# Kernel tuning notes

Hardware: AMD Instinct MI355X
Metric: run time of the kernel (lower is better)

## Reference

```python
import jax, jax.numpy as jnp
import numpy as np

D_MODEL = 1024
N_HEADS = 16
HEAD_DIM = D_MODEL // N_HEADS


def setup_inputs() -> dict:
    key = jax.random.key(0)
    k1, k2, k3 = jax.random.split(key, 3)
    B, S = 4, 2048
    x = jax.random.normal(k1, (B, S, D_MODEL), dtype=jnp.float32)
    # scaled init so logits stay reasonable
    w_qkv = jax.random.normal(k2, (D_MODEL, 3 * D_MODEL), dtype=jnp.float32) / np.sqrt(D_MODEL)
    b_qkv = jnp.zeros((3 * D_MODEL,), dtype=jnp.float32)
    w_out = jax.random.normal(k3, (D_MODEL, D_MODEL), dtype=jnp.float32) / np.sqrt(D_MODEL)
    b_out = jnp.zeros((D_MODEL,), dtype=jnp.float32)
    return {"x": x, "w_qkv": w_qkv, "b_qkv": b_qkv, "w_out": w_out, "b_out": b_out}


def reference(x, w_qkv, b_qkv, w_out, b_out):
    B, S, D = x.shape
    qkv = x @ w_qkv + b_qkv                      # [B,S,3D]
    q, k, v = jnp.split(qkv, 3, axis=-1)
    def split_heads(t):
        return t.reshape(B, S, N_HEADS, HEAD_DIM).transpose(0, 2, 1, 3)  # [B,H,S,d]
    q, k, v = split_heads(q), split_heads(k), split_heads(v)
    a = jnp.einsum('bhsd,bhtd->bhst', q, k)      # [B,H,S,S]
    # causal mask added BEFORE scaling, as in the original module
    causal_mask = jnp.triu(jnp.full((S, S), -jnp.inf, dtype=a.dtype), k=1)
    a = (a + causal_mask) / np.sqrt(HEAD_DIM)
    a = jax.nn.softmax(a, axis=-1)
    z = jnp.einsum('bhst,bhtd->bhsd', a, v)      # [B,H,S,d]
    z = z.transpose(0, 2, 1, 3).reshape(B, S, D)
    return z @ w_out + b_out
```

## Files before the change

### kernel.cpp

```cpp
#include <hip/hip_runtime.h>
#include <hip/hip_bf16.h>
#include <stdint.h>

#define B_   4
#define S_   2048
#define H_   16
#define HD_  64
#define D_   1024

typedef short  short8  __attribute__((ext_vector_type(8)));
typedef float  f32x4   __attribute__((ext_vector_type(4)));
typedef float  f32x16  __attribute__((ext_vector_type(16)));

__device__ __forceinline__ unsigned short f2bf(float f) {
    union { float f; unsigned u; } v; v.f = f;
    unsigned r = v.u + 0x7fffu + ((v.u >> 16) & 1u);
    return (unsigned short)(r >> 16);
}

#if __has_builtin(__builtin_amdgcn_exp2f)
#define EXP2(x) __builtin_amdgcn_exp2f(x)
#else
#define EXP2(x) exp2f(x)
#endif

__device__ __forceinline__ unsigned cvtpk(float lo, float hi) {
    unsigned r;
    asm("v_cvt_pk_bf16_f32 %0, %1, %2" : "=v"(r) : "v"(lo), "v"(hi));
    return r;
}

__device__ __forceinline__ float bq(float v, int srclane) {
    return __int_as_float(__builtin_amdgcn_ds_bpermute(srclane << 2, __float_as_int(v)));
}

__device__ __forceinline__ void pl32swap(unsigned &x, unsigned &y) {
    asm volatile("v_permlane32_swap_b32 %0, %1" : "+v"(x), "+v"(y));
}

#define MFMA32(a, b, c) __builtin_amdgcn_mfma_f32_32x32x16_bf16(a, b, c, 0, 0, 0)
#define MFMA16(a, b, c) __builtin_amdgcn_mfma_f32_16x16x32_bf16(a, b, c, 0, 0, 0)

__global__ __launch_bounds__(256) void k_cvt(const float* __restrict__ in,
                                             unsigned short* __restrict__ out) {
    int i = (blockIdx.x * 256 + threadIdx.x) * 4;
    float4 f = *(const float4*)(in + i);
    ushort4 o;
    o.x = f2bf(f.x); o.y = f2bf(f.y); o.z = f2bf(f.z); o.w = f2bf(f.w);
    *(ushort4*)(out + i) = o;
}

__global__ __launch_bounds__(256) void k_transpose_cvt(const float* __restrict__ in,
                                                       unsigned short* __restrict__ out,
                                                       int K, int N) {
    __shared__ float tile[32][33];
    int n0 = blockIdx.x * 32, k0 = blockIdx.y * 32;
    int tx = threadIdx.x, ty = threadIdx.y;
#pragma unroll
    for (int i = 0; i < 32; i += 8)
        tile[ty + i][tx] = in[(size_t)(k0 + ty + i) * N + n0 + tx];
    __syncthreads();
#pragma unroll
    for (int i = 0; i < 32; i += 8)
        out[(size_t)(n0 + ty + i) * K + k0 + tx] = f2bf(tile[tx][ty + i]);
}

__device__ __forceinline__ void async_load16(const unsigned short* g, unsigned short* l) {
    __builtin_amdgcn_global_load_lds(
        (const __attribute__((address_space(1))) unsigned int*)g,
        (__attribute__((address_space(3))) unsigned int*)l, 16, 0, 0);
}

template <int TPOSED>
__global__ __launch_bounds__(512, 1) void k_gemm8(const unsigned short* __restrict__ A,
                                                  const unsigned short* __restrict__ BT,
                                                  const float* __restrict__ bias,
                                                  unsigned short* __restrict__ qb,
                                                  unsigned short* __restrict__ kb,
                                                  unsigned short* __restrict__ vtb,
                                                  int M, int N, int K, int nbase) {
    __shared__ __attribute__((aligned(16))) unsigned short A0s[256 * 64];
    __shared__ __attribute__((aligned(16))) unsigned short A1s[256 * 64];
    __shared__ __attribute__((aligned(16))) unsigned short A2s[256 * 64];
    __shared__ __attribute__((aligned(16))) unsigned short W0s[128 * 64];
    __shared__ __attribute__((aligned(16))) unsigned short W1s[128 * 64];
    __shared__ __attribute__((aligned(16))) unsigned short W2s[128 * 64];
    const int tid = threadIdx.x, wave = tid >> 6, lane = tid & 63;
    const int wR = wave >> 2, wC = wave & 3;
    const int m0 = blockIdx.y * 256, n0 = nbase + blockIdx.x * 128;

    const unsigned short* AG = A + (size_t)m0 * K;
    const unsigned short* WG = BT + (size_t)n0 * K;

    const int rbase = wave * 8 + (lane >> 3);
    const int scol8 = ((lane & 7) ^ ((lane >> 3) & 7)) * 8;
    const int sdst  = wave * 512;
    const int q15 = lane & 15, q4 = (lane >> 4) << 2;
    const int cb0 = ((lane >> 4) * 16) ^ ((lane & 7) << 4);
    const int cb1 = (64 + (lane >> 4) * 16) ^ ((lane & 7) << 4);

    f32x4 acc[2][4][2] = {};

#define STAGE3(SA, SW, KT, KH)                                                        \
    if ((KH) == 0) {                                                                  \
        async_load16(AG + (size_t)(rbase)       * K + (KT) + scol8, (SA) + 0 * 4096 + sdst); \
        async_load16(AG + (size_t)(64 + rbase)  * K + (KT) + scol8, (SA) + 1 * 4096 + sdst); \
        async_load16(WG + (size_t)(rbase)       * K + (KT) + scol8, (SW) + 0 * 4096 + sdst); \
    } else {                                                                          \
        async_load16(AG + (size_t)(128 + rbase) * K + (KT) + scol8, (SA) + 2 * 4096 + sdst); \
        async_load16(AG + (size_t)(192 + rbase) * K + (KT) + scol8, (SA) + 3 * 4096 + sdst); \
        async_load16(WG + (size_t)(64 + rbase)  * K + (KT) + scol8, (SW) + 1 * 4096 + sdst); \
    }

#define PHASEBODY(CA, CW, SA, SW, MORE, KT2, KH, CB)                                  \
    {                                                                                 \
        short8 xf[2][4], yf[2][2];                                                    \
        if (TPOSED) {                                                                 \
            _Pragma("unroll")                                                         \
            for (int i = 0; i < 4; ++i)                                               \
                xf[0][i] = *(const short8*)((const char*)(CW) + (wR * 64 + i * 16 + q15) * 128 + (CB)); \
            _Pragma("unroll")                                                         \
            for (int h = 0; h < 2; ++h)                                               \
                _Pragma("unroll")                                                     \
                for (int j = 0; j < 2; ++j)                                           \
                    yf[h][j] = *(const short8*)((const char*)(CA) + (h * 128 + wC * 32 + j * 16 + q15) * 128 + (CB)); \
        } else {                                                                      \
            _Pragma("unroll")                                                         \
            for (int h = 0; h < 2; ++h)                                               \
                _Pragma("unroll")                                                     \
                for (int i = 0; i < 4; ++i)                                           \
                    xf[h][i] = *(const short8*)((const char*)(CA) + (h * 128 + wR * 64 + i * 16 + q15) * 128 + (CB)); \
            _Pragma("unroll")                                                         \
            for (int j = 0; j < 2; ++j)                                               \
                yf[0][j] = *(const short8*)((const char*)(CW) + (wC * 32 + j * 16 + q15) * 128 + (CB)); \
        }                                                                             \
        if (MORE) {                                                                   \
            STAGE3(SA, SW, KT2, KH)                                                   \
            asm volatile("s_waitcnt vmcnt(6)" ::: "memory");                          \
        } else {                                                                      \
            asm volatile("s_waitcnt vmcnt(0)" ::: "memory");                          \
        }                                                                             \
        __builtin_amdgcn_s_barrier();                                                 \
        asm volatile("s_waitcnt lgkmcnt(0)" ::: "memory");                            \
        __builtin_amdgcn_sched_barrier(0);                                            \
        __builtin_amdgcn_s_setprio(1);                                                \
        _Pragma("unroll")                                                             \
        for (int h = 0; h < 2; ++h)                                                   \
            _Pragma("unroll")                                                         \
            for (int i = 0; i < 4; ++i)                                               \
                _Pragma("unroll")                                                     \
                for (int j = 0; j < 2; ++j)                                           \
                    acc[h][i][j] = MFMA16(TPOSED ? xf[0][i] : xf[h][i],               \
                                          TPOSED ? yf[h][j] : yf[0][j],               \
                                          acc[h][i][j]);                              \
        __builtin_amdgcn_s_setprio(0);                                                \
        asm volatile("" ::: "memory");                                                \
        __builtin_amdgcn_s_barrier();                                                 \
    }

#define TILEBODY(CA, CW, SA, SW, TC)                                                  \
    {                                                                                 \
        const int more_ = ((TC) + 2) < 16;                                            \
        const int kt2_ = ((TC) + 2) * 64;                                             \
        PHASEBODY(CA, CW, SA, SW, more_, kt2_, 0, cb0)                                \
        PHASEBODY(CA, CW, SA, SW, more_, kt2_, 1, cb1)                                \
    }

    STAGE3(A0s, W0s, 0, 0)
    STAGE3(A0s, W0s, 0, 1)
    STAGE3(A1s, W1s, 64, 0)
    STAGE3(A1s, W1s, 64, 1)
    asm volatile("s_waitcnt vmcnt(6)" ::: "memory");
    __builtin_amdgcn_s_barrier();

    for (int t = 0; t < 15; t += 3) {
        TILEBODY(A0s, W0s, A2s, W2s, t)
        TILEBODY(A1s, W1s, A0s, W0s, t + 1)
        TILEBODY(A2s, W2s, A1s, W1s, t + 2)
    }
    TILEBODY(A0s, W0s, A2s, W2s, 15)
#undef STAGE3
#undef PHASEBODY
#undef TILEBODY

    if (TPOSED) {
        unsigned short* dst = (n0 < 1024) ? qb : kb;
        const float scale = (n0 < 1024) ? 0.18033688011112042f : 1.0f;
#pragma unroll
        for (int i = 0; i < 4; ++i) {
            int nr = n0 + wR * 64 + i * 16 + q4;
            float4 bv4 = *(const float4*)(bias + nr);
            int d0 = nr & 63, hh = (nr & 1023) >> 6;
#pragma unroll
            for (int h = 0; h < 2; ++h)
#pragma unroll
            for (int j = 0; j < 2; ++j) {
                int mc = m0 + h * 128 + wC * 32 + j * 16 + q15;
                int b = mc >> 11, s = mc & 2047;
                size_t bh = (size_t)(b * 16 + hh);
                f32x4 a = acc[h][i][j];
                ushort4 o;
                o.x = f2bf((a[0] + bv4.x) * scale);
                o.y = f2bf((a[1] + bv4.y) * scale);
                o.z = f2bf((a[2] + bv4.z) * scale);
                o.w = f2bf((a[3] + bv4.w) * scale);
                size_t off = bh * 131072 +
                    (size_t)((s >> 5) * 4 + (d0 >> 4)) * 512 +
                    ((s & 31) * 2 + ((d0 >> 3) & 1)) * 8 + (d0 & 7);
                *(ushort4*)(dst + off) = o;
            }
        }
    } else {
#pragma unroll
        for (int h = 0; h < 2; ++h)
#pragma unroll
        for (int i = 0; i < 4; ++i) {
            int mr = m0 + h * 128 + wR * 64 + i * 16 + q4;
            int b = mr >> 11, s0 = mr & 2047;
#pragma unroll
            for (int j = 0; j < 2; ++j) {
                int nc = n0 + wC * 32 + j * 16 + q15;
                int rem = nc & 1023, hh = rem >> 6, d = rem & 63;
                float bv = bias[nc];
                f32x4 a = acc[h][i][j];
                ushort4 o;
                o.x = f2bf(a[0] + bv);
                o.y = f2bf(a[1] + bv);
                o.z = f2bf(a[2] + bv);
                o.w = f2bf(a[3] + bv);
                size_t bh = (size_t)(b * 16 + hh);
                size_t off = bh * 131072 +
                    (size_t)((s0 >> 5) * 4 + (d >> 5) * 2 + ((s0 >> 4) & 1)) * 512 +
                    (((d & 31) << 1) + ((s0 >> 3) & 1)) * 8 + (s0 & 7);
                *(ushort4*)(vtb + off) = o;
            }
        }
    }
}

__global__ __launch_bounds__(512, 1) void k_gemm_out8(const unsigned short* __restrict__ A,
                                                      const unsigned short* __restrict__ BT,
                                                      const float* __restrict__ bias,
                                                      float* __restrict__ outf,
                                                      int M, int N, int K) {
    __shared__ __attribute__((aligned(16))) unsigned short A0s[256 * 64];
    __shared__ __attribute__((aligned(16))) unsigned short A1s[256 * 64];
    __shared__ __attribute__((aligned(16))) unsigned short A2s[256 * 64];
    __shared__ __attribute__((aligned(16))) unsigned short W0s[128 * 64];
    __shared__ __attribute__((aligned(16))) unsigned short W1s[128 * 64];
    __shared__ __attribute__((aligned(16))) unsigned short W2s[128 * 64];
    const int tid = threadIdx.x, wave = tid >> 6, lane = tid & 63;
    const int wR = wave >> 2, wC = wave & 3;
    const int m0 = blockIdx.y * 256, n0 = blockIdx.x * 128;

    const unsigned short* AG = A + (size_t)m0 * K;
    const unsigned short* WG = BT + (size_t)n0 * K;

    const int rbase = wave * 8 + (lane >> 3);
    const int scol8 = ((lane & 7) ^ ((lane >> 3) & 7)) * 8;
    const int sdst  = wave * 512;
    const int q15 = lane & 15, q4 = (lane >> 4) << 2;
    const int cb0 = ((lane >> 4) * 16) ^ ((lane & 7) << 4);
    const int cb1 = (64 + (lane >> 4) * 16) ^ ((lane & 7) << 4);

    f32x4 acc[2][4][2] = {};

#define STAGE3O(SA, SW, KT, KH)                                                       \
    if ((KH) == 0) {                                                                  \
        async_load16(AG + (size_t)(rbase)       * K + (KT) + scol8, (SA) + 0 * 4096 + sdst); \
        async_load16(AG + (size_t)(64 + rbase)  * K + (KT) + scol8, (SA) + 1 * 4096 + sdst); \
        async_load16(WG + (size_t)(rbase)       * K + (KT) + scol8, (SW) + 0 * 4096 + sdst); \
    } else {                                                                          \
        async_load16(AG + (size_t)(128 + rbase) * K + (KT) + scol8, (SA) + 2 * 4096 + sdst); \
        async_load16(AG + (size_t)(192 + rbase) * K + (KT) + scol8, (SA) + 3 * 4096 + sdst); \
        async_load16(WG + (size_t)(64 + rbase)  * K + (KT) + scol8, (SW) + 1 * 4096 + sdst); \
    }

#define PHASEBODYO(CA, CW, SA, SW, MORE, KT2, KH, CB)                                 \
    {                                                                                 \
        short8 xf[4], yf[2][2];                                                       \
        _Pragma("unroll")                                                             \
        for (int i = 0; i < 4; ++i)                                                   \
            xf[i] = *(const short8*)((const char*)(CW) + (wR * 64 + i * 16 + q15) * 128 + (CB)); \
        _Pragma("unroll")                                                             \
        for (int h = 0; h < 2; ++h)                                                   \
            _Pragma("unroll")                                                         \
            for (int j = 0; j < 2; ++j)                                               \
                yf[h][j] = *(const short8*)((const char*)(CA) + (h * 128 + wC * 32 + j * 16 + q15) * 128 + (CB)); \
        if (MORE) {                                                                   \
            STAGE3O(SA, SW, KT2, KH)                                                  \
            asm volatile("s_waitcnt vmcnt(6)" ::: "memory");                          \
        } else {                                                                      \
            asm volatile("s_waitcnt vmcnt(0)" ::: "memory");                          \
        }                                                                             \
        __builtin_amdgcn_s_barrier();                                                 \
        asm volatile("s_waitcnt lgkmcnt(0)" ::: "memory");                            \
        __builtin_amdgcn_sched_barrier(0);                                            \
        __builtin_amdgcn_s_setprio(1);                                                \
        _Pragma("unroll")                                                             \
        for (int h = 0; h < 2; ++h)                                                   \
            _Pragma("unroll")                                                         \
            for (int i = 0; i < 4; ++i)                                               \
                _Pragma("unroll")                                                     \
                for (int j = 0; j < 2; ++j)                                           \
                    acc[h][i][j] = MFMA16(xf[i], yf[h][j], acc[h][i][j]);             \
        __builtin_amdgcn_s_setprio(0);                                                \
        asm volatile("" ::: "memory");                                                \
        __builtin_amdgcn_s_barrier();                                                 \
    }

#define TILEBODYO(CA, CW, SA, SW, TC)                                                 \
    {                                                                                 \
        const int more_ = ((TC) + 2) < 16;                                            \
        const int kt2_ = ((TC) + 2) * 64;                                             \
        PHASEBODYO(CA, CW, SA, SW, more_, kt2_, 0, cb0)                               \
        PHASEBODYO(CA, CW, SA, SW, more_, kt2_, 1, cb1)                               \
    }

    STAGE3O(A0s, W0s, 0, 0)
    STAGE3O(A0s, W0s, 0, 1)
    STAGE3O(A1s, W1s, 64, 0)
    STAGE3O(A1s, W1s, 64, 1)
    asm volatile("s_waitcnt vmcnt(6)" ::: "memory");
    __builtin_amdgcn_s_barrier();

    for (int t = 0; t < 15; t += 3) {
        TILEBODYO(A0s, W0s, A2s, W2s, t)
        TILEBODYO(A1s, W1s, A0s, W0s, t + 1)
        TILEBODYO(A2s, W2s, A1s, W1s, t + 2)
    }
    TILEBODYO(A0s, W0s, A2s, W2s, 15)
#undef STAGE3O
#undef PHASEBODYO
#undef TILEBODYO

#pragma unroll
    for (int i = 0; i < 4; ++i) {
        int nr = n0 + wR * 64 + i * 16 + q4;
        float4 bv4 = *(const float4*)(bias + nr);
#pragma unroll
        for (int h = 0; h < 2; ++h)
#pragma unroll
        for (int j = 0; j < 2; ++j) {
            int mc = m0 + h * 128 + wC * 32 + j * 16 + q15;
            f32x4 a = acc[h][i][j];
            float4 o;
            o.x = a[0] + bv4.x;
            o.y = a[1] + bv4.y;
            o.z = a[2] + bv4.z;
            o.w = a[3] + bv4.w;
            *(float4*)(outf + (size_t)mc * N + nr) = o;
        }
    }
}

__device__ __forceinline__ void do_strip(int strip, int bh, int c, int hi,
                                         const unsigned short* __restrict__ QFb,
                                         const unsigned short* __restrict__ KFb,
                                         const unsigned short* __restrict__ VFb,
                                         unsigned short* __restrict__ Z) {
    const int qbase = strip * 32;
    const int b = bh >> 4, h = bh & 15;
    const int lp8 = ((c << 1) + hi) << 3;

    short8 qf[4];
#pragma unroll
    for (int kd = 0; kd < 4; kd++)
        qf[kd] = *(const short8*)(QFb + (strip * 4 + kd) * 512 + lp8);

    f32x16 o0a = {}, o0b = {}, o1a = {}, o1b = {};
    float l_r = 0.f;
    const int nkv = strip + 1;

    short8 kf_cur[4], kf_nxt[4];
#pragma unroll
    for (int kd = 0; kd < 4; kd++)
        kf_cur[kd] = *(const short8*)(KFb + kd * 512 + lp8);

    for (int tt = 0; tt < nkv; ++tt) {
        const int tn = (tt + 1 < nkv) ? (tt + 1) : tt;
#pragma unroll
        for (int kd = 0; kd < 4; kd++)
            kf_nxt[kd] = *(const short8*)(KFb + (tn * 4 + kd) * 512 + lp8);

        short8 vf[2][2];
#pragma unroll
        for (int dt = 0; dt < 2; dt++)
#pragma unroll
            for (int ks = 0; ks < 2; ks++)
                vf[dt][ks] = *(const short8*)(VFb + (tt * 4 + dt * 2 + ks) * 512 + lp8);

        f32x16 sTa = {}, sTb = {};
        sTa = MFMA32(kf_cur[0], qf[0], sTa);
        sTb = MFMA32(kf_cur[2], qf[2], sTb);
        sTa = MFMA32(kf_cur[1], qf[1], sTa);
        sTb = MFMA32(kf_cur[3], qf[3], sTb);
        f32x16 sT;
#pragma unroll
        for (int r = 0; r < 16; r++) sT[r] = sTa[r] + sTb[r];

        if (tt * 32 == qbase) {
#pragma unroll
            for (int r = 0; r < 16; r++) {
                int tl = (r & 3) + 8 * (r >> 2) + 4 * hi;
                if (tl > c) sT[r] = -1e30f;
            }
        }

#pragma unroll
        for (int r = 0; r < 16; r++) sT[r] = EXP2(sT[r]);
        float s0 = sT[0] + sT[8],  s1 = sT[1] + sT[9];
        float s2 = sT[2] + sT[10], s3 = sT[3] + sT[11];
        float s4 = sT[4] + sT[12], s5 = sT[5] + sT[13];
        float s6 = sT[6] + sT[14], s7 = sT[7] + sT[15];
        s0 += s4; s1 += s5; s2 += s6; s3 += s7;
        l_r += (s0 + s2) + (s1 + s3);

        unsigned pk0 = cvtpk(sT[0],  sT[1]);
        unsigned pk1 = cvtpk(sT[2],  sT[3]);
        unsigned pk2 = cvtpk(sT[4],  sT[5]);
        unsigned pk3 = cvtpk(sT[6],  sT[7]);
        unsigned pk4 = cvtpk(sT[8],  sT[9]);
        unsigned pk5 = cvtpk(sT[10], sT[11]);
        unsigned pk6 = cvtpk(sT[12], sT[13]);
        unsigned pk7 = cvtpk(sT[14], sT[15]);
        pl32swap(pk0, pk2);
        pl32swap(pk1, pk3);
        pl32swap(pk4, pk6);
        pl32swap(pk5, pk7);
        union { unsigned u[4]; short8 s; } pa0, pa1;
        pa0.u[0] = pk0; pa0.u[1] = pk1; pa0.u[2] = pk2; pa0.u[3] = pk3;
        pa1.u[0] = pk4; pa1.u[1] = pk5; pa1.u[2] = pk6; pa1.u[3] = pk7;

        o0a = MFMA32(pa0.s, vf[0][0], o0a);
        o1a = MFMA32(pa0.s, vf[1][0], o1a);
        o0b = MFMA32(pa1.s, vf[0][1], o0b);
        o1b = MFMA32(pa1.s, vf[1][1], o1b);

#pragma unroll
        for (int kd = 0; kd < 4; kd++) kf_cur[kd] = kf_nxt[kd];
    }

    l_r += __shfl_xor(l_r, 32);
    float inv = __builtin_amdgcn_rcpf(l_r);
#pragma unroll
    for (int r = 0; r < 16; r++) {
        int crow = (r & 3) + 8 * (r >> 2) + 4 * hi;
        float ib = bq(inv, crow);
        int q = qbase + crow;
        unsigned short* zp = Z + ((size_t)b * S_ + q) * D_ + h * HD_;
        zp[c]      = f2bf((o0a[r] + o0b[r]) * ib);
        zp[32 + c] = f2bf((o1a[r] + o1b[r]) * ib);
    }
}

__global__ __launch_bounds__(128, 2) void k_attn(const unsigned short* __restrict__ QF,
                                                 const unsigned short* __restrict__ KF,
                                                 const unsigned short* __restrict__ VF,
                                                 unsigned short* __restrict__ Z) {
    const int i = blockIdx.x;
    const int bh = (i & 7) * 8 + ((i >> 3) & 7);
    const int pr = i >> 6;
    const int tid = threadIdx.x;
    const int wave = tid >> 6, lane = tid & 63;
    const int c = lane & 31, hi = lane >> 5;
    const int strip = wave ? (63 - pr) : pr;
    const unsigned short* QFb = QF + (size_t)bh * 131072;
    const unsigned short* KFb = KF + (size_t)bh * 131072;
    const unsigned short* VFb = VF + (size_t)bh * 131072;
    do_strip(strip, bh, c, hi, QFb, KFb, VFb, Z);
}

extern "C" void kernel_launch(void* const* d_in, const int* in_sizes, int n_in,
                              void* d_out, int out_size, void* d_ws, size_t ws_size,
                              hipStream_t stream) {
    const float* x     = (const float*)d_in[0];
    const float* w_qkv = (const float*)d_in[1];
    const float* b_qkv = (const float*)d_in[2];
    const float* w_out = (const float*)d_in[3];
    const float* b_out = (const float*)d_in[4];
    float* out = (float*)d_out;

    char* ws = (char*)d_ws;
    unsigned short* xb    = (unsigned short*)(ws + 0);
    unsigned short* wqkvT = (unsigned short*)(ws + 16777216);
    unsigned short* woutT = (unsigned short*)(ws + 23068672);
    unsigned short* qb    = (unsigned short*)(ws + 25165824);
    unsigned short* kb    = (unsigned short*)(ws + 41943040);
    unsigned short* vtb   = (unsigned short*)(ws + 58720256);
    unsigned short* zb    = xb;

    k_cvt<<<8192, 256, 0, stream>>>(x, xb);
    k_transpose_cvt<<<dim3(96, 32), dim3(32, 8), 0, stream>>>(w_qkv, wqkvT, 1024, 3072);
    k_transpose_cvt<<<dim3(32, 32), dim3(32, 8), 0, stream>>>(w_out, woutT, 1024, 1024);
    k_gemm8<1><<<dim3(16, 32), 512, 0, stream>>>(xb, wqkvT, b_qkv, qb, kb, vtb,
                                                 8192, 3072, 1024, 0);
    k_gemm8<0><<<dim3(8, 32), 512, 0, stream>>>(xb, wqkvT, b_qkv, qb, kb, vtb,
                                                8192, 3072, 1024, 2048);
    k_attn<<<2048, 128, 0, stream>>>(qb, kb, vtb, zb);
    k_gemm_out8<<<dim3(8, 32), 512, 0, stream>>>(zb, woutT, b_out, out, 8192, 1024, 1024);
}
```

Baseline: 169.4 us.

## Split each attention strip's KV range across two waves with LDS reduction

Each attention block now handles a single 32-row query strip, and its two waves each process half of the causal KV tiles. The partial outputs and row sums are combined through shared memory before the normalized bf16 write, and the grid doubles. Blocks are issued longest strip first. The old scheme paired a short and a long strip in one block, so the two waves had unequal lengths; this change aims to balance them and shorten the tail. In exchange it adds a shared-memory round trip, a barrier, and a redundant Q load per wave.

```diff
diff --git a/kernel.cpp b/kernel.cpp
--- a/kernel.cpp
+++ b/kernel.cpp
@@ -354,121 +354,149 @@
     }
 }
 
-__device__ __forceinline__ void do_strip(int strip, int bh, int c, int hi,
-                                         const unsigned short* __restrict__ QFb,
-                                         const unsigned short* __restrict__ KFb,
-                                         const unsigned short* __restrict__ VFb,
-                                         unsigned short* __restrict__ Z) {
-    const int qbase = strip * 32;
-    const int b = bh >> 4, h = bh & 15;
-    const int lp8 = ((c << 1) + hi) << 3;
-
+__device__ __forceinline__ void attn_range(int qbase, int tbeg, int tend,
+                                           int c, int hi, int lp8,
+                                           const unsigned short* __restrict__ QFb,
+                                           const unsigned short* __restrict__ KFb,
+                                           const unsigned short* __restrict__ VFb,
+                                           f32x16& o0, f32x16& o1, float& l_out) {
     short8 qf[4];
 #pragma unroll
     for (int kd = 0; kd < 4; kd++)
-        qf[kd] = *(const short8*)(QFb + (strip * 4 + kd) * 512 + lp8);
+        qf[kd] = *(const short8*)(QFb + ((qbase >> 5) * 4 + kd) * 512 + lp8);
 
     f32x16 o0a = {}, o0b = {}, o1a = {}, o1b = {};
     float l_r = 0.f;
-    const int nkv = strip + 1;
-
-    short8 kf_cur[4], kf_nxt[4];
-#pragma unroll
-    for (int kd = 0; kd < 4; kd++)
-        kf_cur[kd] = *(const short8*)(KFb + kd * 512 + lp8);
-
-    for (int tt = 0; tt < nkv; ++tt) {
-        const int tn = (tt + 1 < nkv) ? (tt + 1) : tt;
+
+    if (tbeg < tend) {
+        short8 kf_cur[4], kf_nxt[4];
 #pragma unroll
         for (int kd = 0; kd < 4; kd++)
-            kf_nxt[kd] = *(const short8*)(KFb + (tn * 4 + kd) * 512 + lp8);
-
-        short8 vf[2][2];
-#pragma unroll
-        for (int dt = 0; dt < 2; dt++)
-#pragma unroll
-            for (int ks = 0; ks < 2; ks++)
-                vf[dt][ks] = *(const short8*)(VFb + (tt * 4 + dt * 2 + ks) * 512 + lp8);
-
-        f32x16 sTa = {}, sTb = {};
-        sTa = MFMA32(kf_cur[0], qf[0], sTa);
-        sTb = MFMA32(kf_cur[2], qf[2], sTb);
-        sTa = MFMA32(kf_cur[1], qf[1], sTa);
-        sTb = MFMA32(kf_cur[3], qf[3], sTb);
-        f32x16 sT;
-#pragma unroll
-        for (int r = 0; r < 16; r++) sT[r] = sTa[r] + sTb[r];
-
-        if (tt * 32 == qbase) {
-#pragma unroll
-            for (int r = 0; r < 16; r++) {
-                int tl = (r & 3) + 8 * (r >> 2) + 4 * hi;
-                if (tl > c) sT[r] = -1e30f;
+            kf_cur[kd] = *(const short8*)(KFb + (tbeg * 4 + kd) * 512 + lp8);
+
+        for (int tt = tbeg; tt < tend; ++tt) {
+            const int tn = (tt + 1 < tend) ? (tt + 1) : tt;
+#pragma unroll
+            for (int kd = 0; kd < 4; kd++)
+                kf_nxt[kd] = *(const short8*)(KFb + (tn * 4 + kd) * 512 + lp8);
+
+            short8 vf[2][2];
+#pragma unroll
+            for (int dt = 0; dt < 2; dt++)
+#pragma unroll
+                for (int ks = 0; ks < 2; ks++)
+                    vf[dt][ks] = *(const short8*)(VFb + (tt * 4 + dt * 2 + ks) * 512 + lp8);
+
+            f32x16 sTa = {}, sTb = {};
+            sTa = MFMA32(kf_cur[0], qf[0], sTa);
+            sTb = MFMA32(kf_cur[2], qf[2], sTb);
+            sTa = MFMA32(kf_cur[1], qf[1], sTa);
+            sTb = MFMA32(kf_cur[3], qf[3], sTb);
+            f32x16 sT;
+#pragma unroll
+            for (int r = 0; r < 16; r++) sT[r] = sTa[r] + sTb[r];
+
+            if (tt * 32 == qbase) {
+#pragma unroll
+                for (int r = 0; r < 16; r++) {
+                    int tl = (r & 3) + 8 * (r >> 2) + 4 * hi;
+                    if (tl > c) sT[r] = -1e30f;
+                }
             }
+
+#pragma unroll
+            for (int r = 0; r < 16; r++) sT[r] = EXP2(sT[r]);
+            float s0 = sT[0] + sT[8],  s1 = sT[1] + sT[9];
+            float s2 = sT[2] + sT[10], s3 = sT[3] + sT[11];
+            float s4 = sT[4] + sT[12], s5 = sT[5] + sT[13];
+            float s6 = sT[6] + sT[14], s7 = sT[7] + sT[15];
+            s0 += s4; s1 += s5; s2 += s6; s3 += s7;
+            l_r += (s0 + s2) + (s1 + s3);
+
+            unsigned pk0 = cvtpk(sT[0],  sT[1]);
+            unsigned pk1 = cvtpk(sT[2],  sT[3]);
+            unsigned pk2 = cvtpk(sT[4],  sT[5]);
+            unsigned pk3 = cvtpk(sT[6],  sT[7]);
+            unsigned pk4 = cvtpk(sT[8],  sT[9]);
+            unsigned pk5 = cvtpk(sT[10], sT[11]);
+            unsigned pk6 = cvtpk(sT[12], sT[13]);
+            unsigned pk7 = cvtpk(sT[14], sT[15]);
+            pl32swap(pk0, pk2);
+            pl32swap(pk1, pk3);
+            pl32swap(pk4, pk6);
+            pl32swap(pk5, pk7);
+            union { unsigned u[4]; short8 s; } pa0, pa1;
+            pa0.u[0] = pk0; pa0.u[1] = pk1; pa0.u[2] = pk2; pa0.u[3] = pk3;
+            pa1.u[0] = pk4; pa1.u[1] = pk5; pa1.u[2] = pk6; pa1.u[3] = pk7;
+
+            o0a = MFMA32(pa0.s, vf[0][0], o0a);
+            o1a = MFMA32(pa0.s, vf[1][0], o1a);
+            o0b = MFMA32(pa1.s, vf[0][1], o0b);
+            o1b = MFMA32(pa1.s, vf[1][1], o1b);
+
+#pragma unroll
+            for (int kd = 0; kd < 4; kd++) kf_cur[kd] = kf_nxt[kd];
         }
-
-#pragma unroll
-        for (int r = 0; r < 16; r++) sT[r] = EXP2(sT[r]);
-        float s0 = sT[0] + sT[8],  s1 = sT[1] + sT[9];
-        float s2 = sT[2] + sT[10], s3 = sT[3] + sT[11];
-        float s4 = sT[4] + sT[12], s5 = sT[5] + sT[13];
-        float s6 = sT[6] + sT[14], s7 = sT[7] + sT[15];
-        s0 += s4; s1 += s5; s2 += s6; s3 += s7;
-        l_r += (s0 + s2) + (s1 + s3);
-
-        unsigned pk0 = cvtpk(sT[0],  sT[1]);
-        unsigned pk1 = cvtpk(sT[2],  sT[3]);
-        unsigned pk2 = cvtpk(sT[4],  sT[5]);
-        unsigned pk3 = cvtpk(sT[6],  sT[7]);
-        unsigned pk4 = cvtpk(sT[8],  sT[9]);
-        unsigned pk5 = cvtpk(sT[10], sT[11]);
-        unsigned pk6 = cvtpk(sT[12], sT[13]);
-        unsigned pk7 = cvtpk(sT[14], sT[15]);
-        pl32swap(pk0, pk2);
-        pl32swap(pk1, pk3);
-        pl32swap(pk4, pk6);
-        pl32swap(pk5, pk7);
-        union { unsigned u[4]; short8 s; } pa0, pa1;
-        pa0.u[0] = pk0; pa0.u[1] = pk1; pa0.u[2] = pk2; pa0.u[3] = pk3;
-        pa1.u[0] = pk4; pa1.u[1] = pk5; pa1.u[2] = pk6; pa1.u[3] = pk7;
-
-        o0a = MFMA32(pa0.s, vf[0][0], o0a);
-        o1a = MFMA32(pa0.s, vf[1][0], o1a);
-        o0b = MFMA32(pa1.s, vf[0][1], o0b);
-        o1b = MFMA32(pa1.s, vf[1][1], o1b);
-
-#pragma unroll
-        for (int kd = 0; kd < 4; kd++) kf_cur[kd] = kf_nxt[kd];
-    }
-
+    }
+
+#pragma unroll
+    for (int r = 0; r < 16; r++) {
+        o0[r] = o0a[r] + o0b[r];
+        o1[r] = o1a[r] + o1b[r];
+    }
     l_r += __shfl_xor(l_r, 32);
-    float inv = __builtin_amdgcn_rcpf(l_r);
-#pragma unroll
-    for (int r = 0; r < 16; r++) {
-        int crow = (r & 3) + 8 * (r >> 2) + 4 * hi;
-        float ib = bq(inv, crow);
-        int q = qbase + crow;
-        unsigned short* zp = Z + ((size_t)b * S_ + q) * D_ + h * HD_;
-        zp[c]      = f2bf((o0a[r] + o0b[r]) * ib);
-        zp[32 + c] = f2bf((o1a[r] + o1b[r]) * ib);
-    }
+    l_out = l_r;
 }
 
 __global__ __launch_bounds__(128, 2) void k_attn(const unsigned short* __restrict__ QF,
                                                  const unsigned short* __restrict__ KF,
                                                  const unsigned short* __restrict__ VF,
                                                  unsigned short* __restrict__ Z) {
+    __shared__ float OL[32][64];
+    __shared__ float lL[32];
+
     const int i = blockIdx.x;
     const int bh = (i & 7) * 8 + ((i >> 3) & 7);
-    const int pr = i >> 6;
+    const int strip = 63 - (i >> 6);
     const int tid = threadIdx.x;
     const int wave = tid >> 6, lane = tid & 63;
     const int c = lane & 31, hi = lane >> 5;
-    const int strip = wave ? (63 - pr) : pr;
+    const int qbase = strip * 32;
+    const int nkv = strip + 1, half = (nkv + 1) >> 1;
+    const int lp8 = ((c << 1) + hi) << 3;
     const unsigned short* QFb = QF + (size_t)bh * 131072;
     const unsigned short* KFb = KF + (size_t)bh * 131072;
     const unsigned short* VFb = VF + (size_t)bh * 131072;
-    do_strip(strip, bh, c, hi, QFb, KFb, VFb, Z);
+
+    f32x16 o0, o1;
+    float l_r;
+    attn_range(qbase, wave ? half : 0, wave ? nkv : half,
+               c, hi, lp8, QFb, KFb, VFb, o0, o1, l_r);
+
+    if (wave) {
+#pragma unroll
+        for (int r = 0; r < 16; r++) {
+            int crow = (r & 3) + 8 * (r >> 2) + 4 * hi;
+            OL[crow][c]      = o0[r];
+            OL[crow][32 + c] = o1[r];
+        }
+        if (hi == 0) lL[c] = l_r;
+    }
+    __syncthreads();
+    if (!wave) {
+        l_r += lL[c];
+        float inv = __builtin_amdgcn_rcpf(l_r);
+        const int b = bh >> 4, h = bh & 15;
+#pragma unroll
+        for (int r = 0; r < 16; r++) {
+            int crow = (r & 3) + 8 * (r >> 2) + 4 * hi;
+            float ib = bq(inv, crow);
+            int q = qbase + crow;
+            unsigned short* zp = Z + ((size_t)b * S_ + q) * D_ + h * HD_;
+            zp[c]      = f2bf((o0[r] + OL[crow][c]) * ib);
+            zp[32 + c] = f2bf((o1[r] + OL[crow][32 + c]) * ib);
+        }
+    }
 }
 
 extern "C" void kernel_launch(void* const* d_in, const int* in_sizes, int n_in,
@@ -497,6 +525,6 @@
                                                  8192, 3072, 1024, 0);
     k_gemm8<0><<<dim3(8, 32), 512, 0, stream>>>(xb, wqkvT, b_qkv, qb, kb, vtb,
                                                 8192, 3072, 1024, 2048);
-    k_attn<<<2048, 128, 0, stream>>>(qb, kb, vtb, zb);
+    k_attn<<<4096, 128, 0, stream>>>(qb, kb, vtb, zb);
     k_gemm_out8<<<dim3(8, 32), 512, 0, stream>>>(zb, woutT, b_out, out, 8192, 1024, 1024);
 }
```

Result: no change. 171.9 us (+1.5%).
